# Performance work log

Measured on AMD Instinct MI355X. Metric: run time of the kernel, lower is better.

Reference implementation:

```python
import jax, jax.numpy as jnp
import numpy as np

B, T, D, H, C = 8, 512, 1024, 16, 10   # batch, seq (T_out+1), d=nb_lon*nb_lat, heads, classes
L = 4                                   # effective layers = n - 1 (ModuleLists hold n-1 entries)
DH = D // H
RD = float(np.sqrt(D))
EPS = 1e-5


def make_pos():
    # pos[t, 2k] = sin((t+1)*w_k), pos[t, 2k+1] = sin((t+1)*w_k + pi/2)
    t = np.arange(1, T + 1, dtype=np.float32)[:, None]          # [T,1]
    kk = np.arange(D // 2, dtype=np.float32)
    omega = np.repeat(1.0 / 1000.0 ** (2.0 * kk / D), 2)[None]  # [1,D]
    phase = np.tile(np.array([0.0, np.pi / 2], dtype=np.float32), D // 2)[None]
    return jnp.asarray(np.sin(t * omega + phase), dtype=jnp.float32)


def setup_inputs() -> dict:
    key = jax.random.key(0)
    ks = jax.random.split(key, 12)
    s = 0.02
    inp = {
        'x': jax.random.normal(ks[0], (B, T, D), jnp.float32),
        'k': jax.random.normal(ks[1], (B, H, T, DH), jnp.float32),
        'v': jax.random.normal(ks[2], (B, H, T, DH), jnp.float32),
        'pos': make_pos(),
        'Wq1': jax.random.normal(ks[3], (L, D, D), jnp.float32) * s,
        'Wk1': jax.random.normal(ks[4], (L, D, D), jnp.float32) * s,
        'Wv1': jax.random.normal(ks[5], (L, D, D), jnp.float32) * s,
        'Wq2': jax.random.normal(ks[6], (L, D, D), jnp.float32) * s,
        'Wfc': jax.random.normal(ks[7], (L, D, D), jnp.float32) * s,
        'bfc': jnp.zeros((L, D), jnp.float32),
        'g1': jnp.ones((L - 1, D), jnp.float32),
        'b1': jnp.zeros((L - 1, D), jnp.float32),
        'g2': jnp.ones((L, D), jnp.float32),
        'b2': jnp.zeros((L, D), jnp.float32),
        'g3': jnp.ones((L, D), jnp.float32),
        'b3': jnp.zeros((L, D), jnp.float32),
        # xavier_uniform on [1, C-1]
        'cutoff': jax.random.uniform(ks[8], (1, C - 1), jnp.float32,
                                     -np.sqrt(6.0 / C), np.sqrt(6.0 / C)),
    }
    return inp


def _ln(x, g, b):
    m = jnp.mean(x, axis=-1, keepdims=True)
    var = jnp.var(x, axis=-1, keepdims=True)
    return (x - m) / jnp.sqrt(var + EPS) * g + b


def _self_attn(x, Wq, Wk, Wv):
    # nn.Linear: y = x @ W.T ; no causal mask (masking defaults to False)
    q = (x @ Wq.T).reshape(B, T, H, DH)
    kk = (x @ Wk.T).reshape(B, T, H, DH)
    vv = (x @ Wv.T).reshape(B, T, H, DH)
    a = jnp.einsum('bqhe,bkhe->bhqk', q, kk) / RD
    a = jax.nn.softmax(a, axis=-1)
    o = jnp.einsum('bhqk,bkhe->bqhe', a, vv).reshape(B, T, D)
    return x + o


def _cross_attn(x, Wq, k, v, mask):
    q = (x @ Wq.T).reshape(B, T, H, DH)
    a = jnp.einsum('bqhe,bhke->bhqk', q, k) / RD
    a = jnp.where(mask, -jnp.inf, a)  # causal mask on cross scores (intended semantics)
    a = jax.nn.softmax(a, axis=-1)
    o = jnp.einsum('bhqk,bhke->bqhe', a, v).reshape(B, T, D)
    return x + o


def reference(x, k, v, pos, Wq1, Wk1, Wv1, Wq2, Wfc, bfc,
              g1, b1, g2, b2, g3, b3, cutoff):
    x = x + pos
    mask = jnp.triu(jnp.ones((T, T), bool), 1)
    for i in range(L):
        if i != 0:
            x = _ln(x, g1[i - 1], b1[i - 1])
        x = _self_attn(x, Wq1[i], Wk1[i], Wv1[i])
        x = _ln(x, g2[i], b2[i])
        x = _cross_attn(x, Wq2[i], k, v, mask)
        x = _ln(x, g3[i], b3[i])
        x = jax.nn.relu(x @ Wfc[i].T + bfc[i]) + x
    # ordinal sigmoid head: cumulative cutoffs, adjacent sigmoid differences
    b = jnp.cumsum(jnp.concatenate([cutoff[:, :1], cutoff[:, 1:] ** 2], axis=1), axis=1)  # [1,C-1]
    sig = jax.nn.sigmoid(b[0] - x[..., None])  # [B,T,D,C-1]
    probs = jnp.concatenate(
        [sig[..., :1], sig[..., 1:] - sig[..., :-1], 1.0 - sig[..., -1:]], axis=-1)
    return probs
```

## Files before the change

kernel.cpp:

```cpp
#include <hip/hip_runtime.h>


#define BB   8
#define TT   512
#define DD   1024
#define HH   16
#define DHH  64
#define LLAY 4
#define MM   (BB*TT)
#define MD   ((size_t)MM*DD)
#define INV_RD (1.0f/32.0f)
#define LNEPS 1e-5f

typedef unsigned short ushort_t;
typedef __attribute__((ext_vector_type(8))) short short8;
typedef __attribute__((ext_vector_type(4))) float floatx4;

__device__ inline ushort_t f2bf(float f) {
  unsigned u = __builtin_bit_cast(unsigned, f);
  unsigned r = (u + 0x7FFFu + ((u >> 16) & 1u)) >> 16;
  return (ushort_t)r;
}

__global__ __launch_bounds__(256) void cast_all_k(
    const float* __restrict__ Wq1, const float* __restrict__ Wk1,
    const float* __restrict__ Wv1, const float* __restrict__ Wq2f,
    const float* __restrict__ Wfcf, const float* __restrict__ kin,
    const float* __restrict__ vin, const float* __restrict__ x,
    const float* __restrict__ pos,
    ushort_t* __restrict__ wqkv, ushort_t* __restrict__ wq2,
    ushort_t* __restrict__ wfc, ushort_t* __restrict__ kinbf,
    ushort_t* __restrict__ vinbf, float* __restrict__ cur,
    ushort_t* __restrict__ act_bf) {
  int seg = blockIdx.x >> 12;
  size_t j = ((size_t)(blockIdx.x & 4095)) * 256 + threadIdx.x;
  if (seg == 7) {
    int dq  = (int)(j & 255);
    int row = (int)(j >> 8);
    int t   = row & (TT - 1);
    float4 a = ((const float4*)x)[j];
    float4 p = ((const float4*)pos)[(size_t)t * 256 + dq];
    a.x += p.x; a.y += p.y; a.z += p.z; a.w += p.w;
    ((float4*)cur)[j] = a;
    ushort4 b; b.x = f2bf(a.x); b.y = f2bf(a.y); b.z = f2bf(a.z); b.w = f2bf(a.w);
    ((ushort4*)act_bf)[j] = b;
    return;
  }
  const float* src;
  switch (seg) {
    case 0: src = Wq1; break;
    case 1: src = Wk1; break;
    case 2: src = Wv1; break;
    case 3: src = Wq2f; break;
    case 4: src = Wfcf; break;
    case 5: src = kin; break;
    default: src = vin; break;
  }
  float4 v = ((const float4*)src)[j];
  ushort4 o; o.x = f2bf(v.x); o.y = f2bf(v.y); o.z = f2bf(v.z); o.w = f2bf(v.w);
  if (seg < 3) {
    int d4 = (int)(j & 255);
    int n  = (int)((j >> 8) & 1023);
    int i  = (int)(j >> 18);
    size_t drow = (size_t)i * 3072 + (size_t)seg * 1024 + n;
    ((ushort4*)wqkv)[drow * 256 + d4] = o;
  } else {
    ushort_t* dst = (seg == 3) ? wq2 : (seg == 4) ? wfc : (seg == 5) ? kinbf : vinbf;
    ((ushort4*)dst)[j] = o;
  }
}

__global__ __launch_bounds__(256) void ln_k(const float* __restrict__ in,
                                            float* __restrict__ out,
                                            ushort_t* __restrict__ out_bf,
                                            const float* __restrict__ g,
                                            const float* __restrict__ bt) {
  int row = blockIdx.x;
  int t = threadIdx.x;
  const float4* r4 = (const float4*)(in + (size_t)row * DD);
  float4 v = r4[t];
  float s  = v.x + v.y + v.z + v.w;
  float ss = v.x*v.x + v.y*v.y + v.z*v.z + v.w*v.w;
#pragma unroll
  for (int off = 32; off > 0; off >>= 1) {
    s  += __shfl_down(s, off);
    ss += __shfl_down(ss, off);
  }
  __shared__ float red[8];
  int w = t >> 6;
  if ((t & 63) == 0) { red[w] = s; red[4 + w] = ss; }
  __syncthreads();
  s  = red[0] + red[1] + red[2] + red[3];
  ss = red[4] + red[5] + red[6] + red[7];
  float mean = s * (1.0f / DD);
  float var  = ss * (1.0f / DD) - mean * mean;
  float inv  = rsqrtf(var + LNEPS);
  float4 gv = ((const float4*)g)[t];
  float4 bv = ((const float4*)bt)[t];
  float4 o;
  o.x = (v.x - mean) * inv * gv.x + bv.x;
  o.y = (v.y - mean) * inv * gv.y + bv.y;
  o.z = (v.z - mean) * inv * gv.z + bv.z;
  o.w = (v.w - mean) * inv * gv.w + bv.w;
  ((float4*)(out + (size_t)row * DD))[t] = o;
  ushort4 ob; ob.x = f2bf(o.x); ob.y = f2bf(o.y); ob.z = f2bf(o.z); ob.w = f2bf(o.w);
  ((ushort4*)(out_bf + (size_t)row * DD))[t] = ob;
}

__global__ __launch_bounds__(256) void gemm_mfma_bt_k(const ushort_t* __restrict__ A,
                                                      const ushort_t* __restrict__ W,
                                                      ushort_t* __restrict__ Cout,
                                                      int nbx) {
  __shared__ ushort_t As[128 * 32];
  __shared__ ushort_t Bs[128 * 32];
  int t = threadIdx.x;
  int d = blockIdx.x;
  int chunk = gridDim.x >> 3;
  int logical = (d & 7) * chunk + (d >> 3);
  int bx = logical % nbx, by = logical / nbx;
  int n0 = bx * 128, m0 = by * 128;
  int lane = t & 63, w = t >> 6;
  int wm = (w >> 1) * 64, wn = (w & 1) * 64;
  int fr = lane & 15, q = lane >> 4;
  const short8* ap[4]; const short8* bp[4];
#pragma unroll
  for (int i = 0; i < 4; i++) {
    int r  = wm + i * 16 + fr;
    int rn = wn + i * 16 + fr;
    ap[i] = (const short8*)(As + r  * 32 + ((q ^ ((r  >> 1) & 3)) * 8));
    bp[i] = (const short8*)(Bs + rn * 32 + ((q ^ ((rn >> 1) & 3)) * 8));
  }
  auto* As3 = (__attribute__((address_space(3))) ushort_t*)As;
  auto* Bs3 = (__attribute__((address_space(3))) ushort_t*)Bs;
  floatx4 acc[4][4] = {};
  for (int k0 = 0; k0 < DD; k0 += 32) {
    __syncthreads();
#pragma unroll
    for (int j = 0; j < 2; j++) {
      int e = t + j * 256;
      int row = e >> 2, slot = e & 3;
      int c = slot ^ ((row >> 1) & 3);
      const ushort_t* asrc = A + (size_t)(m0 + row) * DD + k0 + c * 8;
      const ushort_t* wsrc = W + (size_t)(n0 + row) * DD + k0 + c * 8;
      __builtin_amdgcn_global_load_lds(
          (const __attribute__((address_space(1))) unsigned*)asrc,
          (__attribute__((address_space(3))) unsigned*)(As3 + e * 8), 16, 0, 0);
      __builtin_amdgcn_global_load_lds(
          (const __attribute__((address_space(1))) unsigned*)wsrc,
          (__attribute__((address_space(3))) unsigned*)(Bs3 + e * 8), 16, 0, 0);
    }
    __syncthreads();
    short8 af[4], bf[4];
#pragma unroll
    for (int i = 0; i < 4; i++) { af[i] = *ap[i]; bf[i] = *bp[i]; }
#pragma unroll
    for (int i = 0; i < 4; i++)
#pragma unroll
      for (int j = 0; j < 4; j++)
        acc[i][j] = __builtin_amdgcn_mfma_f32_16x16x32_bf16(af[i], bf[j], acc[i][j], 0, 0, 0);
  }
  int orow = m0 + wm + q * 4;
  int ocol = n0 + wn + fr;
  int seg = n0 >> 10;
  ushort_t* Cb = Cout + (size_t)seg * MD;
#pragma unroll
  for (int i = 0; i < 4; i++)
#pragma unroll
    for (int j = 0; j < 4; j++)
#pragma unroll
      for (int rr = 0; rr < 4; rr++)
        Cb[(size_t)(orow + i * 16 + rr) * DD + ((ocol + j * 16) & 1023)] =
            f2bf(acc[i][j][rr]);
}

__global__ __launch_bounds__(256) void gemm64_k(const ushort_t* __restrict__ A,
                                                const ushort_t* __restrict__ W,
                                                void* __restrict__ Cout,
                                                const float* __restrict__ bias,
                                                const float* __restrict__ lnres,
                                                int mode) {
  __shared__ ushort_t As[128 * 32];
  __shared__ ushort_t Bs[64 * 32];
  int t = threadIdx.x;
  int d = blockIdx.x;
  int logical = (d & 7) * 64 + (d >> 3);
  int bx = logical & 15, by = logical >> 4;
  int n0 = bx * 64, m0 = by * 128;
  int lane = t & 63, w = t >> 6;
  int wm = (w >> 1) * 64, wn = (w & 1) * 32;
  int fr = lane & 15, q = lane >> 4;
  const short8* ap[4]; const short8* bp[2];
#pragma unroll
  for (int i = 0; i < 4; i++) {
    int r = wm + i * 16 + fr;
    ap[i] = (const short8*)(As + r * 32 + ((q ^ ((r >> 1) & 3)) * 8));
  }
#pragma unroll
  for (int j = 0; j < 2; j++) {
    int rn = wn + j * 16 + fr;
    bp[j] = (const short8*)(Bs + rn * 32 + ((q ^ ((rn >> 1) & 3)) * 8));
  }
  auto* As3 = (__attribute__((address_space(3))) ushort_t*)As;
  auto* Bs3 = (__attribute__((address_space(3))) ushort_t*)Bs;
  floatx4 acc[4][2] = {};
  for (int k0 = 0; k0 < DD; k0 += 32) {
    __syncthreads();
#pragma unroll
    for (int j = 0; j < 2; j++) {
      int e = t + j * 256;
      int row = e >> 2, slot = e & 3;
      int c = slot ^ ((row >> 1) & 3);
      const ushort_t* asrc = A + (size_t)(m0 + row) * DD + k0 + c * 8;
      __builtin_amdgcn_global_load_lds(
          (const __attribute__((address_space(1))) unsigned*)asrc,
          (__attribute__((address_space(3))) unsigned*)(As3 + e * 8), 16, 0, 0);
    }
    {
      int e = t;
      int row = e >> 2, slot = e & 3;
      int c = slot ^ ((row >> 1) & 3);
      const ushort_t* wsrc = W + (size_t)(n0 + row) * DD + k0 + c * 8;
      __builtin_amdgcn_global_load_lds(
          (const __attribute__((address_space(1))) unsigned*)wsrc,
          (__attribute__((address_space(3))) unsigned*)(Bs3 + e * 8), 16, 0, 0);
    }
    __syncthreads();
    short8 af[4], bf[2];
#pragma unroll
    for (int i = 0; i < 4; i++) af[i] = *ap[i];
#pragma unroll
    for (int j = 0; j < 2; j++) bf[j] = *bp[j];
#pragma unroll
    for (int i = 0; i < 4; i++)
#pragma unroll
      for (int j = 0; j < 2; j++)
        acc[i][j] = __builtin_amdgcn_mfma_f32_16x16x32_bf16(af[i], bf[j], acc[i][j], 0, 0, 0);
  }
  int orow = m0 + wm + q * 4;
  if (mode == 1) {
    ushort_t* Cb = (ushort_t*)Cout;
#pragma unroll
    for (int i = 0; i < 4; i++)
#pragma unroll
      for (int j = 0; j < 2; j++) {
        int colg = n0 + wn + j * 16 + fr;
#pragma unroll
        for (int rr = 0; rr < 4; rr++)
          Cb[(size_t)(orow + i * 16 + rr) * DD + colg] = f2bf(acc[i][j][rr]);
      }
  } else {
    float* C = (float*)Cout;
#pragma unroll
    for (int j = 0; j < 2; j++) {
      int colg = n0 + wn + j * 16 + fr;
      float bv = bias[colg];
#pragma unroll
      for (int i = 0; i < 4; i++)
#pragma unroll
        for (int rr = 0; rr < 4; rr++) {
          size_t idx = (size_t)(orow + i * 16 + rr) * DD + colg;
          C[idx] = fmaxf(acc[i][j][rr] + bv, 0.f) + lnres[idx];
        }
    }
  }
}

__global__ __launch_bounds__(256) void attn_mfma_k(const ushort_t* __restrict__ Qb,
                                                   const ushort_t* __restrict__ Kb,
                                                   const ushort_t* __restrict__ Vb,
                                                   const float* __restrict__ resid,
                                                   float* __restrict__ out,
                                                   int cross) {
  __shared__ ushort_t Qs[64 * 64];
  __shared__ ushort_t Ks[64 * 64];
  __shared__ ushort_t Vts[64 * 64];
  __shared__ ushort_t Ps[4 * 16 * 64];
  int t = threadIdx.x, lane = t & 63, w = t >> 6;
  int fr = lane & 15, q8 = lane >> 4;
  int dsp = blockIdx.x;
  int logical = (dsp & 7) * 128 + (dsp >> 3);
  int qt = logical & 7, bh = logical >> 3;
  int b = bh >> 4, h = bh & 15;
  size_t qbase = ((size_t)(b * TT + qt * 64)) * DD + h * DHH;
  size_t kvbase; int kvstride;
  if (cross) { kvbase = (size_t)bh * TT * DHH;          kvstride = DHH; }
  else       { kvbase = (size_t)b * TT * DD + h * DHH;  kvstride = DD;  }

  auto* Qs3  = (__attribute__((address_space(3))) ushort_t*)Qs;
  auto* Ks3  = (__attribute__((address_space(3))) ushort_t*)Ks;

#pragma unroll
  for (int j = 0; j < 2; j++) {
    int e = t + j * 256;
    int row = e >> 3, slot = e & 7;
    int c = slot ^ (row & 7);
    const ushort_t* src = Qb + qbase + (size_t)row * DD + c * 8;
    __builtin_amdgcn_global_load_lds(
        (const __attribute__((address_space(1))) unsigned*)src,
        (__attribute__((address_space(3))) unsigned*)(Qs3 + e * 8), 16, 0, 0);
  }
  __syncthreads();

  short8 qf[2];
#pragma unroll
  for (int ks = 0; ks < 2; ks++) {
    int row = w * 16 + fr;
    int slot = (ks * 4 + q8) ^ (row & 7);
    qf[ks] = *(const short8*)(Qs + row * 64 + slot * 8);
  }

  float m_i[4], l_i[4];
  floatx4 o_acc[4] = {};
#pragma unroll
  for (int r = 0; r < 4; r++) { m_i[r] = -1e30f; l_i[r] = 0.f; }

  int nch = cross ? (qt + 1) : 8;
  for (int ch = 0; ch < nch; ch++) {
    __syncthreads();
#pragma unroll
    for (int j = 0; j < 2; j++) {
      int e = t + j * 256;
      int row = e >> 3, slot = e & 7;
      int c = slot ^ (row & 7);
      const ushort_t* src = Kb + kvbase + (size_t)(ch * 64 + row) * kvstride + c * 8;
      __builtin_amdgcn_global_load_lds(
          (const __attribute__((address_space(1))) unsigned*)src,
          (__attribute__((address_space(3))) unsigned*)(Ks3 + e * 8), 16, 0, 0);
    }
    {
      int kp = t & 31, dhg = (t >> 5) * 8;
      const ushort_t* v0 = Vb + kvbase + (size_t)(ch * 64 + 2 * kp) * kvstride + dhg;
      short8 a0 = *(const short8*)v0;
      short8 a1 = *(const short8*)(v0 + kvstride);
#pragma unroll
      for (int j = 0; j < 8; j++) {
        int dh = dhg + j;
        int slot = (kp >> 2) ^ (dh & 7);
        unsigned pk = (unsigned)(unsigned short)a0[j] |
                      ((unsigned)(unsigned short)a1[j] << 16);
        *(unsigned*)(Vts + dh * 64 + slot * 8 + (kp & 3) * 2) = pk;
      }
    }
    __syncthreads();

    floatx4 s[4] = {};
    __builtin_amdgcn_s_setprio(1);
#pragma unroll
    for (int nt = 0; nt < 4; nt++) {
      int key = nt * 16 + fr;
#pragma unroll
      for (int ks = 0; ks < 2; ks++) {
        int slot = (ks * 4 + q8) ^ (key & 7);
        short8 kf = *(const short8*)(Ks + key * 64 + slot * 8);
        s[nt] = __builtin_amdgcn_mfma_f32_16x16x32_bf16(qf[ks], kf, s[nt], 0, 0, 0);
      }
    }
    __builtin_amdgcn_s_setprio(0);
    float sv[4][4];
#pragma unroll
    for (int nt = 0; nt < 4; nt++)
#pragma unroll
      for (int r = 0; r < 4; r++)
        sv[nt][r] = s[nt][r] * INV_RD;
    if (cross && ch == qt) {
#pragma unroll
      for (int nt = 0; nt < 4; nt++) {
        int key_g = ch * 64 + nt * 16 + fr;
#pragma unroll
        for (int r = 0; r < 4; r++) {
          int q_g = qt * 64 + w * 16 + q8 * 4 + r;
          if (key_g > q_g) sv[nt][r] = -1e30f;
        }
      }
    }

    float pv[4][4];
#pragma unroll
    for (int r = 0; r < 4; r++) {
      float mch = fmaxf(fmaxf(sv[0][r], sv[1][r]), fmaxf(sv[2][r], sv[3][r]));
#pragma unroll
      for (int off = 1; off < 16; off <<= 1) mch = fmaxf(mch, __shfl_xor(mch, off));
      float mn = fmaxf(m_i[r], mch);
      float alpha = __expf(m_i[r] - mn);
      m_i[r] = mn;
      float rs = 0.f;
#pragma unroll
      for (int nt = 0; nt < 4; nt++) {
        float pe = __expf(sv[nt][r] - mn);
        pv[nt][r] = pe; rs += pe;
      }
#pragma unroll
      for (int off = 1; off < 16; off <<= 1) rs += __shfl_xor(rs, off);
      l_i[r] = l_i[r] * alpha + rs;
#pragma unroll
      for (int nt = 0; nt < 4; nt++) o_acc[nt][r] *= alpha;
    }

    ushort_t* Pw = Ps + w * 1024;
#pragma unroll
    for (int nt = 0; nt < 4; nt++) {
      int col = nt * 16 + fr;
#pragma unroll
      for (int r = 0; r < 4; r++) {
        int row = q8 * 4 + r;
        int slot = (col >> 3) ^ (row & 7);
        Pw[row * 64 + slot * 8 + (col & 7)] = f2bf(pv[nt][r]);
      }
    }
    short8 pf[2];
#pragma unroll
    for (int ks = 0; ks < 2; ks++) {
      int slot = (ks * 4 + q8) ^ (fr & 7);
      pf[ks] = *(const short8*)(Pw + fr * 64 + slot * 8);
    }
    __builtin_amdgcn_s_setprio(1);
#pragma unroll
    for (int nt = 0; nt < 4; nt++) {
      int dh = nt * 16 + fr;
#pragma unroll
      for (int ks = 0; ks < 2; ks++) {
        int slot = (ks * 4 + q8) ^ (dh & 7);
        short8 vf = *(const short8*)(Vts + dh * 64 + slot * 8);
        o_acc[nt] = __builtin_amdgcn_mfma_f32_16x16x32_bf16(pf[ks], vf, o_acc[nt], 0, 0, 0);
      }
    }
    __builtin_amdgcn_s_setprio(0);
  }

  float invl[4];
#pragma unroll
  for (int r = 0; r < 4; r++) invl[r] = 1.0f / l_i[r];
#pragma unroll
  for (int nt = 0; nt < 4; nt++) {
#pragma unroll
    for (int r = 0; r < 4; r++) {
      size_t row_g = (size_t)(b * TT + qt * 64 + w * 16 + q8 * 4 + r);
      size_t idx = row_g * DD + h * DHH + nt * 16 + fr;
      out[idx] = resid[idx] + o_acc[nt][r] * invl[r];
    }
  }
}

__global__ __launch_bounds__(256) void head_k(const float* __restrict__ x,
                                              const float* __restrict__ cut,
                                              float* __restrict__ out) {
  __shared__ float obuf[2560];
  int t = threadIdx.x;
  size_t e = (size_t)blockIdx.x * 256 + t;
  float xv = x[e];
  float bj = cut[0];
  float sprev = 1.0f / (1.0f + __expf(xv - bj));
  obuf[t * 10 + 0] = sprev;
#pragma unroll
  for (int j = 1; j < 9; j++) {
    float cj = cut[j];
    bj += cj * cj;
    float sj = 1.0f / (1.0f + __expf(xv - bj));
    obuf[t * 10 + j] = sj - sprev;
    sprev = sj;
  }
  obuf[t * 10 + 9] = 1.0f - sprev;
  __syncthreads();
  size_t base = (size_t)blockIdx.x * 2560;
#pragma unroll
  for (int r = 0; r < 10; r++) out[base + r * 256 + t] = obuf[r * 256 + t];
}

extern "C" void kernel_launch(void* const* d_in, const int* in_sizes, int n_in,
                              void* d_out, int out_size, void* d_ws, size_t ws_size,
                              hipStream_t stream) {
  (void)in_sizes; (void)n_in; (void)out_size; (void)ws_size;
  const float* x    = (const float*)d_in[0];
  const float* kin  = (const float*)d_in[1];
  const float* vin  = (const float*)d_in[2];
  const float* pos  = (const float*)d_in[3];
  const float* Wq1  = (const float*)d_in[4];
  const float* Wk1  = (const float*)d_in[5];
  const float* Wv1  = (const float*)d_in[6];
  const float* Wq2  = (const float*)d_in[7];
  const float* Wfc  = (const float*)d_in[8];
  const float* bfc  = (const float*)d_in[9];
  const float* g1   = (const float*)d_in[10];
  const float* b1   = (const float*)d_in[11];
  const float* g2   = (const float*)d_in[12];
  const float* b2   = (const float*)d_in[13];
  const float* g3   = (const float*)d_in[14];
  const float* b3   = (const float*)d_in[15];
  const float* cut  = (const float*)d_in[16];
  float* out = (float*)d_out;

  float* cur = (float*)d_ws;
  float* tmp = cur + MD;
  ushort_t* act_bf = (ushort_t*)(tmp + MD);
  ushort_t* qbf    = act_bf + MD;
  ushort_t* kbf    = qbf + MD;
  ushort_t* vbf    = kbf + MD;
  ushort_t* kinbf  = vbf + MD;
  ushort_t* vinbf  = kinbf + MD;
  ushort_t* wqkv   = vinbf + MD;
  ushort_t* wq2    = wqkv + (size_t)LLAY * 3 * DD * DD;
  ushort_t* wfc    = wq2  + (size_t)LLAY * DD * DD;

  dim3 b256(256);

  cast_all_k<<<8 * 4096, b256, 0, stream>>>(Wq1, Wk1, Wv1, Wq2, Wfc, kin, vin,
                                            x, pos, wqkv, wq2, wfc, kinbf, vinbf,
                                            cur, act_bf);

  for (int i = 0; i < LLAY; i++) {
    const float* attn_in;
    if (i) {
      ln_k<<<MM, b256, 0, stream>>>(cur, tmp, act_bf,
                                    g1 + (size_t)(i - 1) * DD, b1 + (size_t)(i - 1) * DD);
      attn_in = tmp;
    } else {
      attn_in = cur;
    }
    gemm_mfma_bt_k<<<768, b256, 0, stream>>>(act_bf, wqkv + (size_t)i * 3 * DD * DD,
                                             qbf, 24);
    attn_mfma_k<<<1024, b256, 0, stream>>>(qbf, kbf, vbf, attn_in, cur, 0);

    ln_k<<<MM, b256, 0, stream>>>(cur, tmp, act_bf,
                                  g2 + (size_t)i * DD, b2 + (size_t)i * DD);
    gemm64_k<<<512, b256, 0, stream>>>(act_bf, wq2 + (size_t)i * DD * DD,
                                       qbf, nullptr, nullptr, 1);
    attn_mfma_k<<<1024, b256, 0, stream>>>(qbf, kinbf, vinbf, tmp, cur, 1);

    ln_k<<<MM, b256, 0, stream>>>(cur, tmp, act_bf,
                                  g3 + (size_t)i * DD, b3 + (size_t)i * DD);
    gemm64_k<<<512, b256, 0, stream>>>(act_bf, wfc + (size_t)i * DD * DD,
                                       cur, bfc + (size_t)i * DD, tmp, 2);
  }

  head_k<<<MD / 256, b256, 0, stream>>>(cur, cut, out);
}
```

Before: 978.9 us.

## Fuse ordinal head into final FC GEMM epilogue and widen attention KV chunks

Measured after the change: 979.6 us. Within noise of the previous version (+0.1%).

```diff
diff --git a/kernel.cpp b/kernel.cpp
--- a/kernel.cpp
+++ b/kernel.cpp
@@ -178,6 +178,7 @@
                                                 void* __restrict__ Cout,
                                                 const float* __restrict__ bias,
                                                 const float* __restrict__ lnres,
+                                                const float* __restrict__ cutv,
                                                 int mode) {
   __shared__ ushort_t As[128 * 32];
   __shared__ ushort_t Bs[64 * 32];
@@ -248,7 +249,7 @@
         for (int rr = 0; rr < 4; rr++)
           Cb[(size_t)(orow + i * 16 + rr) * DD + colg] = f2bf(acc[i][j][rr]);
       }
-  } else {
+  } else if (mode == 2) {
     float* C = (float*)Cout;
 #pragma unroll
     for (int j = 0; j < 2; j++) {
@@ -260,6 +261,37 @@
         for (int rr = 0; rr < 4; rr++) {
           size_t idx = (size_t)(orow + i * 16 + rr) * DD + colg;
           C[idx] = fmaxf(acc[i][j][rr] + bv, 0.f) + lnres[idx];
+        }
+    }
+  } else {
+    float* H = (float*)Cout;
+    float bcum[9];
+    bcum[0] = cutv[0];
+#pragma unroll
+    for (int j = 1; j < 9; j++) { float c = cutv[j]; bcum[j] = bcum[j - 1] + c * c; }
+#pragma unroll
+    for (int j = 0; j < 2; j++) {
+      int colg = n0 + wn + j * 16 + fr;
+      float bv = bias[colg];
+#pragma unroll
+      for (int i = 0; i < 4; i++)
+#pragma unroll
+        for (int rr = 0; rr < 4; rr++) {
+          size_t idx = (size_t)(orow + i * 16 + rr) * DD + colg;
+          float xv = fmaxf(acc[i][j][rr] + bv, 0.f) + lnres[idx];
+          float ov[10];
+          float sp = 1.0f / (1.0f + __expf(xv - bcum[0]));
+          ov[0] = sp;
+#pragma unroll
+          for (int c = 1; c < 9; c++) {
+            float sc = 1.0f / (1.0f + __expf(xv - bcum[c]));
+            ov[c] = sc - sp;
+            sp = sc;
+          }
+          ov[9] = 1.0f - sp;
+          float2* op = (float2*)(H + idx * 10);
+#pragma unroll
+          for (int c = 0; c < 5; c++) { float2 p; p.x = ov[2 * c]; p.y = ov[2 * c + 1]; op[c] = p; }
         }
     }
   }
@@ -271,10 +303,9 @@
                                                    const float* __restrict__ resid,
                                                    float* __restrict__ out,
                                                    int cross) {
-  __shared__ ushort_t Qs[64 * 64];
-  __shared__ ushort_t Ks[64 * 64];
-  __shared__ ushort_t Vts[64 * 64];
-  __shared__ ushort_t Ps[4 * 16 * 64];
+  __shared__ ushort_t Ks[128 * 64];
+  __shared__ ushort_t Vts[64 * 128];
+  __shared__ ushort_t QP[64 * 64];
   int t = threadIdx.x, lane = t & 63, w = t >> 6;
   int fr = lane & 15, q8 = lane >> 4;
   int dsp = blockIdx.x;
@@ -286,8 +317,8 @@
   if (cross) { kvbase = (size_t)bh * TT * DHH;          kvstride = DHH; }
   else       { kvbase = (size_t)b * TT * DD + h * DHH;  kvstride = DD;  }
 
-  auto* Qs3  = (__attribute__((address_space(3))) ushort_t*)Qs;
-  auto* Ks3  = (__attribute__((address_space(3))) ushort_t*)Ks;
+  auto* QP3 = (__attribute__((address_space(3))) ushort_t*)QP;
+  auto* Ks3 = (__attribute__((address_space(3))) ushort_t*)Ks;
 
 #pragma unroll
   for (int j = 0; j < 2; j++) {
@@ -297,7 +328,7 @@
     const ushort_t* src = Qb + qbase + (size_t)row * DD + c * 8;
     __builtin_amdgcn_global_load_lds(
         (const __attribute__((address_space(1))) unsigned*)src,
-        (__attribute__((address_space(3))) unsigned*)(Qs3 + e * 8), 16, 0, 0);
+        (__attribute__((address_space(3))) unsigned*)(QP3 + e * 8), 16, 0, 0);
   }
   __syncthreads();
 
@@ -306,7 +337,7 @@
   for (int ks = 0; ks < 2; ks++) {
     int row = w * 16 + fr;
     int slot = (ks * 4 + q8) ^ (row & 7);
-    qf[ks] = *(const short8*)(Qs + row * 64 + slot * 8);
+    qf[ks] = *(const short8*)(QP + row * 64 + slot * 8);
   }
 
   float m_i[4], l_i[4];
@@ -314,39 +345,44 @@
 #pragma unroll
   for (int r = 0; r < 4; r++) { m_i[r] = -1e30f; l_i[r] = 0.f; }
 
-  int nch = cross ? (qt + 1) : 8;
+  int nch = cross ? ((qt * 64 + 64 + 127) >> 7) : (TT / 128);
   for (int ch = 0; ch < nch; ch++) {
     __syncthreads();
 #pragma unroll
-    for (int j = 0; j < 2; j++) {
+    for (int j = 0; j < 4; j++) {
       int e = t + j * 256;
       int row = e >> 3, slot = e & 7;
       int c = slot ^ (row & 7);
-      const ushort_t* src = Kb + kvbase + (size_t)(ch * 64 + row) * kvstride + c * 8;
+      const ushort_t* src = Kb + kvbase + (size_t)(ch * 128 + row) * kvstride + c * 8;
       __builtin_amdgcn_global_load_lds(
           (const __attribute__((address_space(1))) unsigned*)src,
           (__attribute__((address_space(3))) unsigned*)(Ks3 + e * 8), 16, 0, 0);
     }
     {
       int kp = t & 31, dhg = (t >> 5) * 8;
-      const ushort_t* v0 = Vb + kvbase + (size_t)(ch * 64 + 2 * kp) * kvstride + dhg;
+      const ushort_t* v0 = Vb + kvbase + (size_t)(ch * 128 + 4 * kp) * kvstride + dhg;
       short8 a0 = *(const short8*)v0;
       short8 a1 = *(const short8*)(v0 + kvstride);
+      short8 a2 = *(const short8*)(v0 + 2 * kvstride);
+      short8 a3 = *(const short8*)(v0 + 3 * kvstride);
 #pragma unroll
       for (int j = 0; j < 8; j++) {
         int dh = dhg + j;
-        int slot = (kp >> 2) ^ (dh & 7);
-        unsigned pk = (unsigned)(unsigned short)a0[j] |
-                      ((unsigned)(unsigned short)a1[j] << 16);
-        *(unsigned*)(Vts + dh * 64 + slot * 8 + (kp & 3) * 2) = pk;
+        int slot = (kp >> 1) ^ (dh & 15);
+        unsigned p01 = (unsigned)(unsigned short)a0[j] |
+                       ((unsigned)(unsigned short)a1[j] << 16);
+        unsigned p23 = (unsigned)(unsigned short)a2[j] |
+                       ((unsigned)(unsigned short)a3[j] << 16);
+        uint2 pk; pk.x = p01; pk.y = p23;
+        *(uint2*)(Vts + dh * 128 + slot * 8 + (kp & 1) * 4) = pk;
       }
     }
     __syncthreads();
 
-    floatx4 s[4] = {};
+    floatx4 s[8] = {};
     __builtin_amdgcn_s_setprio(1);
 #pragma unroll
-    for (int nt = 0; nt < 4; nt++) {
+    for (int nt = 0; nt < 8; nt++) {
       int key = nt * 16 + fr;
 #pragma unroll
       for (int ks = 0; ks < 2; ks++) {
@@ -356,16 +392,16 @@
       }
     }
     __builtin_amdgcn_s_setprio(0);
-    float sv[4][4];
-#pragma unroll
-    for (int nt = 0; nt < 4; nt++)
+    float sv[8][4];
+#pragma unroll
+    for (int nt = 0; nt < 8; nt++)
 #pragma unroll
       for (int r = 0; r < 4; r++)
         sv[nt][r] = s[nt][r] * INV_RD;
-    if (cross && ch == qt) {
-#pragma unroll
-      for (int nt = 0; nt < 4; nt++) {
-        int key_g = ch * 64 + nt * 16 + fr;
+    if (cross && ch == nch - 1) {
+#pragma unroll
+      for (int nt = 0; nt < 8; nt++) {
+        int key_g = ch * 128 + nt * 16 + fr;
 #pragma unroll
         for (int r = 0; r < 4; r++) {
           int q_g = qt * 64 + w * 16 + q8 * 4 + r;
@@ -374,10 +410,10 @@
       }
     }
 
-    float pv[4][4];
 #pragma unroll
     for (int r = 0; r < 4; r++) {
-      float mch = fmaxf(fmaxf(sv[0][r], sv[1][r]), fmaxf(sv[2][r], sv[3][r]));
+      float mch = fmaxf(fmaxf(fmaxf(sv[0][r], sv[1][r]), fmaxf(sv[2][r], sv[3][r])),
+                        fmaxf(fmaxf(sv[4][r], sv[5][r]), fmaxf(sv[6][r], sv[7][r])));
 #pragma unroll
       for (int off = 1; off < 16; off <<= 1) mch = fmaxf(mch, __shfl_xor(mch, off));
       float mn = fmaxf(m_i[r], mch);
@@ -385,9 +421,9 @@
       m_i[r] = mn;
       float rs = 0.f;
 #pragma unroll
-      for (int nt = 0; nt < 4; nt++) {
+      for (int nt = 0; nt < 8; nt++) {
         float pe = __expf(sv[nt][r] - mn);
-        pv[nt][r] = pe; rs += pe;
+        sv[nt][r] = pe; rs += pe;
       }
 #pragma unroll
       for (int off = 1; off < 16; off <<= 1) rs += __shfl_xor(rs, off);
@@ -396,35 +432,38 @@
       for (int nt = 0; nt < 4; nt++) o_acc[nt][r] *= alpha;
     }
 
-    ushort_t* Pw = Ps + w * 1024;
-#pragma unroll
-    for (int nt = 0; nt < 4; nt++) {
-      int col = nt * 16 + fr;
-#pragma unroll
-      for (int r = 0; r < 4; r++) {
-        int row = q8 * 4 + r;
-        int slot = (col >> 3) ^ (row & 7);
-        Pw[row * 64 + slot * 8 + (col & 7)] = f2bf(pv[nt][r]);
-      }
-    }
-    short8 pf[2];
-#pragma unroll
-    for (int ks = 0; ks < 2; ks++) {
-      int slot = (ks * 4 + q8) ^ (fr & 7);
-      pf[ks] = *(const short8*)(Pw + fr * 64 + slot * 8);
-    }
-    __builtin_amdgcn_s_setprio(1);
-#pragma unroll
-    for (int nt = 0; nt < 4; nt++) {
-      int dh = nt * 16 + fr;
+    ushort_t* Pw = QP + w * 1024;
+#pragma unroll
+    for (int hf = 0; hf < 2; hf++) {
+#pragma unroll
+      for (int n4 = 0; n4 < 4; n4++) {
+        int col = n4 * 16 + fr;
+#pragma unroll
+        for (int r = 0; r < 4; r++) {
+          int row = q8 * 4 + r;
+          int slot = (col >> 3) ^ (row & 7);
+          Pw[row * 64 + slot * 8 + (col & 7)] = f2bf(sv[hf * 4 + n4][r]);
+        }
+      }
+      short8 pf[2];
 #pragma unroll
       for (int ks = 0; ks < 2; ks++) {
-        int slot = (ks * 4 + q8) ^ (dh & 7);
-        short8 vf = *(const short8*)(Vts + dh * 64 + slot * 8);
-        o_acc[nt] = __builtin_amdgcn_mfma_f32_16x16x32_bf16(pf[ks], vf, o_acc[nt], 0, 0, 0);
-      }
-    }
-    __builtin_amdgcn_s_setprio(0);
+        int slot = (ks * 4 + q8) ^ (fr & 7);
+        pf[ks] = *(const short8*)(Pw + fr * 64 + slot * 8);
+      }
+      __builtin_amdgcn_s_setprio(1);
+#pragma unroll
+      for (int dnt = 0; dnt < 4; dnt++) {
+        int dh = dnt * 16 + fr;
+#pragma unroll
+        for (int ks = 0; ks < 2; ks++) {
+          int vslot = (hf * 8 + ks * 4 + q8) ^ (dh & 15);
+          short8 vf = *(const short8*)(Vts + dh * 128 + vslot * 8);
+          o_acc[dnt] = __builtin_amdgcn_mfma_f32_16x16x32_bf16(pf[ks], vf, o_acc[dnt], 0, 0, 0);
+        }
+      }
+      __builtin_amdgcn_s_setprio(0);
+    }
   }
 
   float invl[4];
@@ -439,31 +478,6 @@
       out[idx] = resid[idx] + o_acc[nt][r] * invl[r];
     }
   }
-}
-
-__global__ __launch_bounds__(256) void head_k(const float* __restrict__ x,
-                                              const float* __restrict__ cut,
-                                              float* __restrict__ out) {
-  __shared__ float obuf[2560];
-  int t = threadIdx.x;
-  size_t e = (size_t)blockIdx.x * 256 + t;
-  float xv = x[e];
-  float bj = cut[0];
-  float sprev = 1.0f / (1.0f + __expf(xv - bj));
-  obuf[t * 10 + 0] = sprev;
-#pragma unroll
-  for (int j = 1; j < 9; j++) {
-    float cj = cut[j];
-    bj += cj * cj;
-    float sj = 1.0f / (1.0f + __expf(xv - bj));
-    obuf[t * 10 + j] = sj - sprev;
-    sprev = sj;
-  }
-  obuf[t * 10 + 9] = 1.0f - sprev;
-  __syncthreads();
-  size_t base = (size_t)blockIdx.x * 2560;
-#pragma unroll
-  for (int r = 0; r < 10; r++) out[base + r * 256 + t] = obuf[r * 256 + t];
 }
 
 extern "C" void kernel_launch(void* const* d_in, const int* in_sizes, int n_in,
@@ -523,14 +537,17 @@
     ln_k<<<MM, b256, 0, stream>>>(cur, tmp, act_bf,
                                   g2 + (size_t)i * DD, b2 + (size_t)i * DD);
     gemm64_k<<<512, b256, 0, stream>>>(act_bf, wq2 + (size_t)i * DD * DD,
-                                       qbf, nullptr, nullptr, 1);
+                                       qbf, nullptr, nullptr, nullptr, 1);
     attn_mfma_k<<<1024, b256, 0, stream>>>(qbf, kinbf, vinbf, tmp, cur, 1);
 
     ln_k<<<MM, b256, 0, stream>>>(cur, tmp, act_bf,
                                   g3 + (size_t)i * DD, b3 + (size_t)i * DD);
-    gemm64_k<<<512, b256, 0, stream>>>(act_bf, wfc + (size_t)i * DD * DD,
-                                       cur, bfc + (size_t)i * DD, tmp, 2);
-  }
-
-  head_k<<<MD / 256, b256, 0, stream>>>(cur, cut, out);
-}
+    if (i < LLAY - 1) {
+      gemm64_k<<<512, b256, 0, stream>>>(act_bf, wfc + (size_t)i * DD * DD,
+                                         cur, bfc + (size_t)i * DD, tmp, nullptr, 2);
+    } else {
+      gemm64_k<<<512, b256, 0, stream>>>(act_bf, wfc + (size_t)i * DD * DD,
+                                         out, bfc + (size_t)i * DD, tmp, cut, 3);
+    }
+  }
+}
```
